# Optimization experiments

Hardware: AMD Instinct MI355X
Metric: run time of the kernel (lower is better)

## Reference

```python
import jax, jax.numpy as jnp
import numpy as np

N_NODES = 100000
N_EDGES = 1600000
NFEAT = 128
NHID = 128
NCLASS = 16


def _sage_conv(x, src, dst, w_self, w_neigh, b):
    # mean aggregation over in-neighbors: for each dst, mean of x[src]
    msgs = x[src]                                   # [E, F] gather
    agg = jax.ops.segment_sum(msgs, dst, num_segments=x.shape[0])  # [N, F]
    deg = jax.ops.segment_sum(jnp.ones((src.shape[0],), x.dtype), dst,
                              num_segments=x.shape[0])             # [N]
    h_neigh = agg / jnp.maximum(deg, 1.0)[:, None]
    return x @ w_self + h_neigh @ w_neigh + b


def setup_inputs() -> dict:
    key = jax.random.key(0)
    ks = jax.random.split(key, 9)
    x = jax.random.normal(ks[0], (N_NODES, NFEAT), dtype=jnp.float32)
    src = jax.random.randint(ks[1], (N_EDGES,), 0, N_NODES, dtype=jnp.int32)
    dst = jax.random.randint(ks[2], (N_EDGES,), 0, N_NODES, dtype=jnp.int32)
    s1 = 1.0 / np.sqrt(NFEAT)
    s2 = 1.0 / np.sqrt(NHID)
    w_self1 = jax.random.uniform(ks[3], (NFEAT, NHID), jnp.float32, -s1, s1)
    w_neigh1 = jax.random.uniform(ks[4], (NFEAT, NHID), jnp.float32, -s1, s1)
    b1 = jnp.zeros((NHID,), jnp.float32)
    w_self2 = jax.random.uniform(ks[5], (NHID, NCLASS), jnp.float32, -s2, s2)
    w_neigh2 = jax.random.uniform(ks[6], (NHID, NCLASS), jnp.float32, -s2, s2)
    b2 = jnp.zeros((NCLASS,), jnp.float32)
    return {"x": x, "src": src, "dst": dst,
            "w_self1": w_self1, "w_neigh1": w_neigh1, "b1": b1,
            "w_self2": w_self2, "w_neigh2": w_neigh2, "b2": b2}


def reference(x, src, dst, w_self1, w_neigh1, b1, w_self2, w_neigh2, b2):
    h = jax.nn.relu(_sage_conv(x, src, dst, w_self1, w_neigh1, b1))
    # dropout is identity in eval mode (training=False)
    out = _sage_conv(h, src, dst, w_self2, w_neigh2, b2)
    return jax.nn.log_softmax(out, axis=1)
```

## Files before the change

### kernel.cpp

```cpp
#include <hip/hip_runtime.h>
#include <math.h>

#define NN 100000
#define NE 1600000
#define BSZ 64
#define NBUCK ((NN + BSZ - 1) / BSZ)
#define NBLK 256
#define CHUNK ((NE + NBLK - 1) / NBLK)
#define NH (NBUCK * NBLK)
#define NSB ((NH + 1023) / 1024)

typedef unsigned int uint;
typedef unsigned short ushort_t;
typedef float f32x2 __attribute__((ext_vector_type(2)));
typedef float f32x4 __attribute__((ext_vector_type(4)));
typedef short s16x8 __attribute__((ext_vector_type(8)));

union U4S8 { uint4 u; s16x8 s; };

__device__ inline uint bf16_1(float f) {
  uint u = __float_as_uint(f);
  return (u + 0x7FFFu + ((u >> 16) & 1u)) >> 16;
}
__device__ inline uint bf16_2(float lo, float hi) {
  return bf16_1(lo) | (bf16_1(hi) << 16);
}
__device__ inline float blo(uint u) { return __uint_as_float(u << 16); }
__device__ inline float bhi(uint u) { return __uint_as_float(u & 0xFFFF0000u); }

__device__ inline f32x4 mfma_bf16(uint4 a, uint4 b, f32x4 c) {
  U4S8 ua, ub; ua.u = a; ub.u = b;
  return __builtin_amdgcn_mfma_f32_16x16x32_bf16(ua.s, ub.s, c, 0, 0, 0);
}

__global__ __launch_bounds__(256) void tobf16_kernel(
    const float* __restrict__ x, uint* __restrict__ xh,
    uint* __restrict__ xq) {
  int i = blockIdx.x * 256 + threadIdx.x;
  if (i >= NN * 16) return;
  const float4* p = (const float4*)x + (size_t)i * 2;
  float4 a = p[0], b = p[1];
  uint4 o;
  o.x = bf16_2(a.x, a.y);
  o.y = bf16_2(a.z, a.w);
  o.z = bf16_2(b.x, b.y);
  o.w = bf16_2(b.z, b.w);
  ((uint4*)xh)[i] = o;
  int q0 = __builtin_amdgcn_cvt_pk_fp8_f32(a.x, a.y, 0, false);
  q0 = __builtin_amdgcn_cvt_pk_fp8_f32(a.z, a.w, q0, true);
  int q1 = __builtin_amdgcn_cvt_pk_fp8_f32(b.x, b.y, 0, false);
  q1 = __builtin_amdgcn_cvt_pk_fp8_f32(b.z, b.w, q1, true);
  uint2 oq; oq.x = (uint)q0; oq.y = (uint)q1;
  int r = i >> 4;
  int u = (i & 15) * 2;
  *(uint2*)(xq + (size_t)r * 32 + u) = oq;
}

__global__ __launch_bounds__(256) void prep_w_kernel(
    const float* __restrict__ ws1, const float* __restrict__ wn1,
    const float* __restrict__ ws2, const float* __restrict__ wn2,
    uint* __restrict__ w1t, uint* __restrict__ w2t) {
  int idx = blockIdx.x * 256 + threadIdx.x;
  if (idx < 128 * 128) {
    int col = idx >> 7, ku = idx & 127;
    int k = ku * 2;
    const float* w = (k < 128) ? ws1 : wn1;
    int kk = (k < 128) ? k : (k - 128);
    w1t[idx] = bf16_2(w[(size_t)kk * 128 + col], w[(size_t)(kk + 1) * 128 + col]);
  } else if (idx < 128 * 128 + 32 * 64) {
    int j = idx - 128 * 128;
    int col = j >> 6, ku = j & 63;
    int k = ku * 2;
    const float* w = (col < 16) ? ws2 : wn2;
    int c = col & 15;
    w2t[j] = bf16_2(w[(size_t)k * 16 + c], w[(size_t)(k + 1) * 16 + c]);
  }
}

__global__ __launch_bounds__(1024) void histA_kernel(
    const int* __restrict__ dst, int* __restrict__ hist2) {
  __shared__ int lh[NBUCK];
  int tid = threadIdx.x;
  int b = blockIdx.x;
  for (int i = tid; i < NBUCK; i += 1024) lh[i] = 0;
  __syncthreads();
  int e0 = b * CHUNK, e1 = min(e0 + CHUNK, NE);
  for (int e = e0 + tid; e < e1; e += 1024) {
    atomicAdd(&lh[dst[e] >> 6], 1);
  }
  __syncthreads();
  for (int i = tid; i < NBUCK; i += 1024)
    hist2[(size_t)b * NBUCK + i] = lh[i];
}

__global__ __launch_bounds__(1024) void transpose_kernel(
    const int* __restrict__ hist2, int* __restrict__ hist) {
  __shared__ int t[32][33];
  int tx = threadIdx.x & 31, ty = threadIdx.x >> 5;
  int i = blockIdx.x * 32 + tx;
  int b = blockIdx.y * 32 + ty;
  if (i < NBUCK) t[ty][tx] = hist2[(size_t)b * NBUCK + i];
  __syncthreads();
  int i2 = blockIdx.x * 32 + ty;
  int b2 = blockIdx.y * 32 + tx;
  if (i2 < NBUCK) hist[(size_t)i2 * NBLK + b2] = t[tx][ty];
}

__global__ __launch_bounds__(1024) void scan_sums_kernel(
    const int* __restrict__ hist, int* __restrict__ sums) {
  __shared__ int sdata[1024];
  int i = blockIdx.x * 1024 + threadIdx.x;
  sdata[threadIdx.x] = (i < NH) ? hist[i] : 0;
  __syncthreads();
#pragma unroll
  for (int s = 512; s > 0; s >>= 1) {
    if (threadIdx.x < s) sdata[threadIdx.x] += sdata[threadIdx.x + s];
    __syncthreads();
  }
  if (threadIdx.x == 0) sums[blockIdx.x] = sdata[0];
}

__global__ __launch_bounds__(512) void scan_tops_kernel(int* __restrict__ sums) {
  __shared__ int buf[2][512];
  int tid = threadIdx.x;
  int v = (tid < NSB) ? sums[tid] : 0;
  buf[0][tid] = v;
  __syncthreads();
  int pp = 0;
#pragma unroll
  for (int d = 1; d < 512; d <<= 1) {
    buf[pp ^ 1][tid] = buf[pp][tid] + ((tid >= d) ? buf[pp][tid - d] : 0);
    pp ^= 1;
    __syncthreads();
  }
  if (tid < NSB) sums[tid] = buf[pp][tid] - v;
}

__global__ __launch_bounds__(1024) void scan_apply_kernel(
    int* __restrict__ hist, const int* __restrict__ sums) {
  __shared__ int buf[2][1024];
  int tid = threadIdx.x;
  int i = blockIdx.x * 1024 + tid;
  int v = (i < NH) ? hist[i] : 0;
  buf[0][tid] = v;
  __syncthreads();
  int pp = 0;
#pragma unroll
  for (int d = 1; d < 1024; d <<= 1) {
    buf[pp ^ 1][tid] = buf[pp][tid] + ((tid >= d) ? buf[pp][tid - d] : 0);
    pp ^= 1;
    __syncthreads();
  }
  if (i < NH) hist[i] = sums[blockIdx.x] + buf[pp][tid] - v;
}

__global__ __launch_bounds__(1024) void scatter3_kernel(
    const int* __restrict__ src, const int* __restrict__ dst,
    const int* __restrict__ scanned, unsigned int* __restrict__ ebuf) {
  __shared__ int cur[NBUCK];
  int tid = threadIdx.x;
  int b = blockIdx.x;
  for (int i = tid; i < NBUCK; i += 1024) cur[i] = scanned[i * NBLK + b];
  __syncthreads();
  int e0 = b * CHUNK, e1 = min(e0 + CHUNK, NE);
  for (int e = e0 + tid; e < e1; e += 1024) {
    int d = dst[e];
    int p = atomicAdd(&cur[d >> 6], 1);
    ebuf[p] = ((unsigned int)(d & 63) << 17) | (unsigned int)src[e];
  }
}

__global__ __launch_bounds__(256) void bucket_sort_kernel(
    const unsigned int* __restrict__ ebuf, const int* __restrict__ scanned,
    int* __restrict__ deg, int* __restrict__ off, int* __restrict__ perm) {
  __shared__ int cnt[BSZ];
  __shared__ int loc_off[BSZ];
  int tid = threadIdx.x;
  int b = blockIdx.x;
  int e0 = scanned[b * NBLK];
  int e1 = (b + 1 < NBUCK) ? scanned[(b + 1) * NBLK] : NE;

  if (tid < BSZ) cnt[tid] = 0;
  __syncthreads();
  for (int e = e0 + tid; e < e1; e += 256)
    atomicAdd(&cnt[ebuf[e] >> 17], 1);
  __syncthreads();

  if (tid < BSZ) {
    int v = cnt[tid];
    int incl = v;
#pragma unroll
    for (int d = 1; d < 64; d <<= 1) {
      int t = __shfl_up(incl, d);
      if (tid >= d) incl += t;
    }
    int excl = incl - v;
    loc_off[tid] = e0 + excl;
    int node = b * BSZ + tid;
    if (node < NN) { off[node] = e0 + excl; deg[node] = v; }
    cnt[tid] = 0;
  }
  __syncthreads();

  for (int e = e0 + tid; e < e1; e += 256) {
    unsigned int pk = ebuf[e];
    int dl = pk >> 17;
    int p = loc_off[dl] + atomicAdd(&cnt[dl], 1);
    perm[p] = (int)(pk & 0x1FFFF);
  }
}

__global__ __launch_bounds__(256) void mean1_kernel(
    const uint* __restrict__ xq, const int* __restrict__ off,
    const int* __restrict__ deg, const int* __restrict__ perm,
    uint* __restrict__ m1h) {
  int node = blockIdx.x * 4 + (threadIdx.x >> 6);
  int lane = threadIdx.x & 63;
  if (node >= NN) return;
  int o = off[node], dg = deg[node];
  int slot = lane >> 5;
  int q = lane & 31;
  f32x2 a0 = {0.f, 0.f}, a1 = {0.f, 0.f};
  int j = 0;
  for (; j + 8 <= dg; j += 8) {
    int sA = perm[o + j + slot];
    int sB = perm[o + j + 2 + slot];
    int sC = perm[o + j + 4 + slot];
    int sD = perm[o + j + 6 + slot];
    uint vA = xq[(size_t)sA * 32 + q];
    uint vB = xq[(size_t)sB * 32 + q];
    uint vC = xq[(size_t)sC * 32 + q];
    uint vD = xq[(size_t)sD * 32 + q];
    a0 += __builtin_amdgcn_cvt_pk_f32_fp8(vA, 0);
    a1 += __builtin_amdgcn_cvt_pk_f32_fp8(vA, 1);
    a0 += __builtin_amdgcn_cvt_pk_f32_fp8(vB, 0);
    a1 += __builtin_amdgcn_cvt_pk_f32_fp8(vB, 1);
    a0 += __builtin_amdgcn_cvt_pk_f32_fp8(vC, 0);
    a1 += __builtin_amdgcn_cvt_pk_f32_fp8(vC, 1);
    a0 += __builtin_amdgcn_cvt_pk_f32_fp8(vD, 0);
    a1 += __builtin_amdgcn_cvt_pk_f32_fp8(vD, 1);
  }
  for (; j + 2 <= dg; j += 2) {
    int s = perm[o + j + slot];
    uint v = xq[(size_t)s * 32 + q];
    a0 += __builtin_amdgcn_cvt_pk_f32_fp8(v, 0);
    a1 += __builtin_amdgcn_cvt_pk_f32_fp8(v, 1);
  }
  if (j < dg && slot == 0) {
    int s = perm[o + j];
    uint v = xq[(size_t)s * 32 + q];
    a0 += __builtin_amdgcn_cvt_pk_f32_fp8(v, 0);
    a1 += __builtin_amdgcn_cvt_pk_f32_fp8(v, 1);
  }
  a0.x += __shfl_xor(a0.x, 32);
  a0.y += __shfl_xor(a0.y, 32);
  a1.x += __shfl_xor(a1.x, 32);
  a1.y += __shfl_xor(a1.y, 32);
  if (slot == 0) {
    float rd = 1.0f / fmaxf((float)dg, 1.0f);
    uint2 o2;
    o2.x = bf16_2(a0.x * rd, a0.y * rd);
    o2.y = bf16_2(a1.x * rd, a1.y * rd);
    *(uint2*)(m1h + (size_t)node * 64 + q * 2) = o2;
  }
}

__global__ __launch_bounds__(256) void gemm12_kernel(
    const uint* __restrict__ xh, const uint* __restrict__ m1h,
    const uint* __restrict__ w1t, const uint* __restrict__ w2t,
    const float* __restrict__ b1, float* __restrict__ oself,
    ushort_t* __restrict__ h2b) {
  __shared__ uint lds_w[128 * 128];
  int tid = threadIdx.x;

#pragma unroll
  for (int i = 0; i < 16; i++) {
    int g = tid + i * 256;
    int row = g >> 5, c = g & 31;
    uint4 v = ((const uint4*)w1t)[g];
    int cs = c ^ (row & 7);
    *(uint4*)&lds_w[row * 128 + cs * 4] = v;
  }
  __syncthreads();

  int wv = tid >> 6;
  int lane = tid & 63;
  int lr = lane & 15, lk = lane >> 4;
  int r0 = blockIdx.x * 256 + wv * 64;

  f32x4 acc[4][8];
#pragma unroll
  for (int i = 0; i < 4; i++)
#pragma unroll
    for (int j = 0; j < 8; j++) acc[i][j] = (f32x4){0.f, 0.f, 0.f, 0.f};

#pragma unroll
  for (int ks = 0; ks < 8; ks++) {
    const uint* A = (ks < 4) ? xh : m1h;
    int ku = (ks & 3) * 16 + lk * 4;
    uint4 a[4];
#pragma unroll
    for (int rt = 0; rt < 4; rt++) {
      int row = r0 + rt * 16 + lr;
      if (row >= NN) row = NN - 1;
      a[rt] = *(const uint4*)(A + (size_t)row * 64 + ku);
    }
    int cbase = ks * 4 + lk;
#pragma unroll
    for (int ct = 0; ct < 8; ct++) {
      int brow = ct * 16 + lr;
      int cs = cbase ^ (lr & 7);
      uint4 bu = *(const uint4*)&lds_w[brow * 128 + cs * 4];
#pragma unroll
      for (int rt = 0; rt < 4; rt++)
        acc[rt][ct] = mfma_bf16(a[rt], bu, acc[rt][ct]);
    }
  }

  float bias[8];
#pragma unroll
  for (int ct = 0; ct < 8; ct++) bias[ct] = b1[ct * 16 + lr];

  __syncthreads();

  ushort_t* lds_h = (ushort_t*)lds_w;
#pragma unroll
  for (int rt = 0; rt < 4; rt++) {
#pragma unroll
    for (int r = 0; r < 4; r++) {
      int rel = wv * 64 + rt * 16 + lk * 4 + r;
#pragma unroll
      for (int ct = 0; ct < 8; ct++) {
        int col = ct * 16 + lr;
        float v = fmaxf(acc[rt][ct][r] + bias[ct], 0.0f);
        int chunk = col >> 3;
        int cs = chunk ^ ((rel & 7) << 1);
        lds_h[rel * 128 + (cs << 3) + (col & 7)] = (ushort_t)bf16_1(v);
      }
    }
  }

  f32x4 acc2[4][2];
#pragma unroll
  for (int i = 0; i < 4; i++)
#pragma unroll
    for (int j = 0; j < 2; j++) acc2[i][j] = (f32x4){0.f, 0.f, 0.f, 0.f};

#pragma unroll
  for (int ks = 0; ks < 4; ks++) {
    uint4 a[4];
#pragma unroll
    for (int rt = 0; rt < 4; rt++) {
      int rel = wv * 64 + rt * 16 + lr;
      int chunk = ks * 4 + lk;
      int cs = chunk ^ ((rel & 7) << 1);
      a[rt] = *(const uint4*)&lds_h[rel * 128 + (cs << 3)];
    }
#pragma unroll
    for (int ct = 0; ct < 2; ct++) {
      uint4 bu = *(const uint4*)(w2t + (size_t)(ct * 16 + lr) * 64 + ks * 16 + lk * 4);
      acc2[0][ct] = mfma_bf16(a[0], bu, acc2[0][ct]);
      acc2[1][ct] = mfma_bf16(a[1], bu, acc2[1][ct]);
      acc2[2][ct] = mfma_bf16(a[2], bu, acc2[2][ct]);
      acc2[3][ct] = mfma_bf16(a[3], bu, acc2[3][ct]);
    }
  }

#pragma unroll
  for (int rt = 0; rt < 4; rt++) {
#pragma unroll
    for (int r = 0; r < 4; r++) {
      int row = r0 + rt * 16 + lk * 4 + r;
      if (row < NN) {
        oself[(size_t)row * 16 + lr] = acc2[rt][0][r];
        h2b[(size_t)row * 16 + lr]  = (ushort_t)bf16_1(acc2[rt][1][r]);
      }
    }
  }
}

__global__ __launch_bounds__(256) void mean2_kernel(
    const ushort_t* __restrict__ h2b, const int* __restrict__ off,
    const int* __restrict__ deg, const int* __restrict__ perm,
    const float* __restrict__ oself, const float* __restrict__ b2,
    float* __restrict__ out) {
  int node = blockIdx.x * 4 + (threadIdx.x >> 6);
  int lane = threadIdx.x & 63;
  if (node >= NN) return;
  int o = off[node], dg = deg[node];
  int slot = lane >> 3;
  int q = lane & 7;
  const uint* hb = (const uint*)h2b;
  float a0 = 0.f, a1 = 0.f;
  int j = slot;
  for (; j + 8 < dg; j += 16) {
    int sA = perm[o + j];
    int sB = perm[o + j + 8];
    uint vA = hb[(size_t)sA * 8 + q];
    uint vB = hb[(size_t)sB * 8 + q];
    a0 += blo(vA) + blo(vB);
    a1 += bhi(vA) + bhi(vB);
  }
  if (j < dg) {
    int s = perm[o + j];
    uint v = hb[(size_t)s * 8 + q];
    a0 += blo(v);
    a1 += bhi(v);
  }
#pragma unroll
  for (int d = 8; d <= 32; d <<= 1) {
    a0 += __shfl_xor(a0, d);
    a1 += __shfl_xor(a1, d);
  }
  float rd = 1.0f / fmaxf((float)dg, 1.0f);
  float2 ob = *(const float2*)(b2 + q * 2);
  float2 os = *(const float2*)(oself + (size_t)node * 16 + q * 2);
  float l0 = os.x + ob.x + a0 * rd;
  float l1 = os.y + ob.y + a1 * rd;
  float m = fmaxf(l0, l1);
#pragma unroll
  for (int d = 1; d <= 4; d <<= 1) m = fmaxf(m, __shfl_xor(m, d));
  float s = __expf(l0 - m) + __expf(l1 - m);
#pragma unroll
  for (int d = 1; d <= 4; d <<= 1) s += __shfl_xor(s, d);
  if (slot == 0) {
    float ls = logf(s);
    float2 r;
    r.x = l0 - m - ls;
    r.y = l1 - m - ls;
    *(float2*)(out + (size_t)node * 16 + q * 2) = r;
  }
}

extern "C" void kernel_launch(void* const* d_in, const int* in_sizes, int n_in,
                              void* d_out, int out_size, void* d_ws, size_t ws_size,
                              hipStream_t stream) {
  const float* x   = (const float*)d_in[0];
  const int*   src = (const int*)d_in[1];
  const int*   dst = (const int*)d_in[2];
  const float* ws1 = (const float*)d_in[3];
  const float* wn1 = (const float*)d_in[4];
  const float* b1  = (const float*)d_in[5];
  const float* ws2 = (const float*)d_in[6];
  const float* wn2 = (const float*)d_in[7];
  const float* b2  = (const float*)d_in[8];
  float* out = (float*)d_out;

  char* p = (char*)d_ws;
  int* deg   = (int*)p;  p += (size_t)NN * 4;
  int* off   = (int*)p;  p += (size_t)NN * 4;
  int* hist  = (int*)p;  p += (size_t)NH * 4;
  int* hist2 = (int*)p;  p += (size_t)NH * 4;
  int* sums  = (int*)p;  p += (size_t)((NSB + 31) & ~31) * 4;
  unsigned int* ebuf = (unsigned int*)p; p += (size_t)NE * 4;
  int* perm = (int*)p;  p += (size_t)NE * 4;
  uint* xh   = (uint*)p; p += (size_t)NN * 64 * 4;
  uint* m1h  = (uint*)p; p += (size_t)NN * 64 * 4;
  uint* xq   = (uint*)p; p += (size_t)NN * 32 * 4;
  uint* w1t  = (uint*)p; p += (size_t)128 * 128 * 4;
  uint* w2t  = (uint*)p; p += (size_t)32 * 64 * 4;
  ushort_t* h2b = (ushort_t*)p; p += (size_t)NN * 16 * 2;
  float* osf    = (float*)p;    p += (size_t)NN * 16 * 4;

  tobf16_kernel<<<(NN * 16 + 255) / 256, 256, 0, stream>>>(x, xh, xq);
  prep_w_kernel<<<(128 * 128 + 32 * 64 + 255) / 256, 256, 0, stream>>>(
      ws1, wn1, ws2, wn2, w1t, w2t);

  histA_kernel<<<NBLK, 1024, 0, stream>>>(dst, hist2);
  transpose_kernel<<<dim3((NBUCK + 31) / 32, NBLK / 32), 1024, 0, stream>>>(
      hist2, hist);
  scan_sums_kernel<<<NSB, 1024, 0, stream>>>(hist, sums);
  scan_tops_kernel<<<1, 512, 0, stream>>>(sums);
  scan_apply_kernel<<<NSB, 1024, 0, stream>>>(hist, sums);
  scatter3_kernel<<<NBLK, 1024, 0, stream>>>(src, dst, hist, ebuf);
  bucket_sort_kernel<<<NBUCK, 256, 0, stream>>>(ebuf, hist, deg, off, perm);

  mean1_kernel<<<(NN + 3) / 4, 256, 0, stream>>>(xq, off, deg, perm, m1h);

  gemm12_kernel<<<(NN + 255) / 256, 256, 0, stream>>>(
      xh, m1h, w1t, w2t, b1, osf, h2b);

  mean2_kernel<<<(NN + 3) / 4, 256, 0, stream>>>(h2b, off, deg, perm, osf, b2, out);
}
```

Measured before the change: 170.1 us.

## Merge prep kernels, load GEMM weights via global_load_lds, process two row tiles per block

Combines the x conversion and weight-prep kernels into a single launch, removing one kernel launch. The gemm12 kernel now loads the weight matrix straight into LDS with global_load_lds, using a pre-swizzled source address, instead of staging it through registers. Each block now handles 512 rows in two halves, which halves the grid. It reloads W1 into LDS between the halves because the LDS buffer is reused for the hidden activations. The fewer blocks reduce per-block fixed overhead but may lower occupancy and parallelism, and the extra syncs and reload add cost.

After: 169.7 us. No clear change (-0.2%).

```diff
diff --git a/kernel.cpp b/kernel.cpp
--- a/kernel.cpp
+++ b/kernel.cpp
@@ -33,47 +33,45 @@
   return __builtin_amdgcn_mfma_f32_16x16x32_bf16(ua.s, ub.s, c, 0, 0, 0);
 }
 
-__global__ __launch_bounds__(256) void tobf16_kernel(
-    const float* __restrict__ x, uint* __restrict__ xh,
-    uint* __restrict__ xq) {
-  int i = blockIdx.x * 256 + threadIdx.x;
-  if (i >= NN * 16) return;
-  const float4* p = (const float4*)x + (size_t)i * 2;
-  float4 a = p[0], b = p[1];
-  uint4 o;
-  o.x = bf16_2(a.x, a.y);
-  o.y = bf16_2(a.z, a.w);
-  o.z = bf16_2(b.x, b.y);
-  o.w = bf16_2(b.z, b.w);
-  ((uint4*)xh)[i] = o;
-  int q0 = __builtin_amdgcn_cvt_pk_fp8_f32(a.x, a.y, 0, false);
-  q0 = __builtin_amdgcn_cvt_pk_fp8_f32(a.z, a.w, q0, true);
-  int q1 = __builtin_amdgcn_cvt_pk_fp8_f32(b.x, b.y, 0, false);
-  q1 = __builtin_amdgcn_cvt_pk_fp8_f32(b.z, b.w, q1, true);
-  uint2 oq; oq.x = (uint)q0; oq.y = (uint)q1;
-  int r = i >> 4;
-  int u = (i & 15) * 2;
-  *(uint2*)(xq + (size_t)r * 32 + u) = oq;
-}
-
-__global__ __launch_bounds__(256) void prep_w_kernel(
+__global__ __launch_bounds__(256) void prep_kernel(
+    const float* __restrict__ x, uint* __restrict__ xh, uint* __restrict__ xq,
     const float* __restrict__ ws1, const float* __restrict__ wn1,
     const float* __restrict__ ws2, const float* __restrict__ wn2,
     uint* __restrict__ w1t, uint* __restrict__ w2t) {
-  int idx = blockIdx.x * 256 + threadIdx.x;
-  if (idx < 128 * 128) {
-    int col = idx >> 7, ku = idx & 127;
-    int k = ku * 2;
-    const float* w = (k < 128) ? ws1 : wn1;
-    int kk = (k < 128) ? k : (k - 128);
-    w1t[idx] = bf16_2(w[(size_t)kk * 128 + col], w[(size_t)(kk + 1) * 128 + col]);
-  } else if (idx < 128 * 128 + 32 * 64) {
-    int j = idx - 128 * 128;
-    int col = j >> 6, ku = j & 63;
-    int k = ku * 2;
-    const float* w = (col < 16) ? ws2 : wn2;
-    int c = col & 15;
-    w2t[j] = bf16_2(w[(size_t)k * 16 + c], w[(size_t)(k + 1) * 16 + c]);
+  int i = blockIdx.x * 256 + threadIdx.x;
+  if (i < NN * 16) {
+    const float4* p = (const float4*)x + (size_t)i * 2;
+    float4 a = p[0], b = p[1];
+    uint4 o;
+    o.x = bf16_2(a.x, a.y);
+    o.y = bf16_2(a.z, a.w);
+    o.z = bf16_2(b.x, b.y);
+    o.w = bf16_2(b.z, b.w);
+    ((uint4*)xh)[i] = o;
+    int q0 = __builtin_amdgcn_cvt_pk_fp8_f32(a.x, a.y, 0, false);
+    q0 = __builtin_amdgcn_cvt_pk_fp8_f32(a.z, a.w, q0, true);
+    int q1 = __builtin_amdgcn_cvt_pk_fp8_f32(b.x, b.y, 0, false);
+    q1 = __builtin_amdgcn_cvt_pk_fp8_f32(b.z, b.w, q1, true);
+    uint2 oq; oq.x = (uint)q0; oq.y = (uint)q1;
+    int r = i >> 4;
+    int u = (i & 15) * 2;
+    *(uint2*)(xq + (size_t)r * 32 + u) = oq;
+  } else {
+    int idx = i - NN * 16;
+    if (idx < 128 * 128) {
+      int col = idx >> 7, ku = idx & 127;
+      int k = ku * 2;
+      const float* w = (k < 128) ? ws1 : wn1;
+      int kk = (k < 128) ? k : (k - 128);
+      w1t[idx] = bf16_2(w[(size_t)kk * 128 + col], w[(size_t)(kk + 1) * 128 + col]);
+    } else if (idx < 128 * 128 + 32 * 64) {
+      int j = idx - 128 * 128;
+      int col = j >> 6, ku = j & 63;
+      int k = ku * 2;
+      const float* w = (col < 16) ? ws2 : wn2;
+      int c = col & 15;
+      w2t[j] = bf16_2(w[(size_t)k * 16 + c], w[(size_t)(k + 1) * 16 + c]);
+    }
   }
 }
 
@@ -272,109 +270,127 @@
     ushort_t* __restrict__ h2b) {
   __shared__ uint lds_w[128 * 128];
   int tid = threadIdx.x;
-
-#pragma unroll
-  for (int i = 0; i < 16; i++) {
-    int g = tid + i * 256;
-    int row = g >> 5, c = g & 31;
-    uint4 v = ((const uint4*)w1t)[g];
-    int cs = c ^ (row & 7);
-    *(uint4*)&lds_w[row * 128 + cs * 4] = v;
-  }
-  __syncthreads();
-
   int wv = tid >> 6;
   int lane = tid & 63;
+
+  {
+#pragma unroll
+    for (int i = 0; i < 16; i++) {
+      int g = tid + i * 256;
+      int row = g >> 5, cs = g & 31;
+      int gsrc = row * 32 + (cs ^ (row & 7));
+      __builtin_amdgcn_global_load_lds(
+          (const uint*)((const uint4*)w1t + gsrc),
+          &lds_w[(size_t)(wv * 64 + i * 256) * 4], 16, 0, 0);
+    }
+  }
+  __syncthreads();
+
   int lr = lane & 15, lk = lane >> 4;
-  int r0 = blockIdx.x * 256 + wv * 64;
-
-  f32x4 acc[4][8];
-#pragma unroll
-  for (int i = 0; i < 4; i++)
-#pragma unroll
-    for (int j = 0; j < 8; j++) acc[i][j] = (f32x4){0.f, 0.f, 0.f, 0.f};
-
-#pragma unroll
-  for (int ks = 0; ks < 8; ks++) {
-    const uint* A = (ks < 4) ? xh : m1h;
-    int ku = (ks & 3) * 16 + lk * 4;
-    uint4 a[4];
+  float bias[8];
+#pragma unroll
+  for (int ct = 0; ct < 8; ct++) bias[ct] = b1[ct * 16 + lr];
+
+  for (int half = 0; half < 2; half++) {
+    int r0 = blockIdx.x * 512 + half * 256 + wv * 64;
+
+    f32x4 acc[4][8];
+#pragma unroll
+    for (int i = 0; i < 4; i++)
+#pragma unroll
+      for (int j = 0; j < 8; j++) acc[i][j] = (f32x4){0.f, 0.f, 0.f, 0.f};
+
+#pragma unroll
+    for (int ks = 0; ks < 8; ks++) {
+      const uint* A = (ks < 4) ? xh : m1h;
+      int ku = (ks & 3) * 16 + lk * 4;
+      uint4 a[4];
+#pragma unroll
+      for (int rt = 0; rt < 4; rt++) {
+        int row = r0 + rt * 16 + lr;
+        if (row >= NN) row = NN - 1;
+        a[rt] = *(const uint4*)(A + (size_t)row * 64 + ku);
+      }
+      int cbase = ks * 4 + lk;
+#pragma unroll
+      for (int ct = 0; ct < 8; ct++) {
+        int brow = ct * 16 + lr;
+        int cs = cbase ^ (lr & 7);
+        uint4 bu = *(const uint4*)&lds_w[brow * 128 + cs * 4];
+#pragma unroll
+        for (int rt = 0; rt < 4; rt++)
+          acc[rt][ct] = mfma_bf16(a[rt], bu, acc[rt][ct]);
+      }
+    }
+
+    __syncthreads();
+    ushort_t* lds_h = (ushort_t*)lds_w;
 #pragma unroll
     for (int rt = 0; rt < 4; rt++) {
-      int row = r0 + rt * 16 + lr;
-      if (row >= NN) row = NN - 1;
-      a[rt] = *(const uint4*)(A + (size_t)row * 64 + ku);
-    }
-    int cbase = ks * 4 + lk;
-#pragma unroll
-    for (int ct = 0; ct < 8; ct++) {
-      int brow = ct * 16 + lr;
-      int cs = cbase ^ (lr & 7);
-      uint4 bu = *(const uint4*)&lds_w[brow * 128 + cs * 4];
-#pragma unroll
-      for (int rt = 0; rt < 4; rt++)
-        acc[rt][ct] = mfma_bf16(a[rt], bu, acc[rt][ct]);
-    }
-  }
-
-  float bias[8];
-#pragma unroll
-  for (int ct = 0; ct < 8; ct++) bias[ct] = b1[ct * 16 + lr];
-
-  __syncthreads();
-
-  ushort_t* lds_h = (ushort_t*)lds_w;
-#pragma unroll
-  for (int rt = 0; rt < 4; rt++) {
-#pragma unroll
-    for (int r = 0; r < 4; r++) {
-      int rel = wv * 64 + rt * 16 + lk * 4 + r;
-#pragma unroll
-      for (int ct = 0; ct < 8; ct++) {
-        int col = ct * 16 + lr;
-        float v = fmaxf(acc[rt][ct][r] + bias[ct], 0.0f);
-        int chunk = col >> 3;
+#pragma unroll
+      for (int r = 0; r < 4; r++) {
+        int rel = wv * 64 + rt * 16 + lk * 4 + r;
+#pragma unroll
+        for (int ct = 0; ct < 8; ct++) {
+          int col = ct * 16 + lr;
+          float v = fmaxf(acc[rt][ct][r] + bias[ct], 0.0f);
+          int chunk = col >> 3;
+          int cs = chunk ^ ((rel & 7) << 1);
+          lds_h[rel * 128 + (cs << 3) + (col & 7)] = (ushort_t)bf16_1(v);
+        }
+      }
+    }
+
+    f32x4 acc2[4][2];
+#pragma unroll
+    for (int i = 0; i < 4; i++)
+#pragma unroll
+      for (int j = 0; j < 2; j++) acc2[i][j] = (f32x4){0.f, 0.f, 0.f, 0.f};
+
+#pragma unroll
+    for (int ks = 0; ks < 4; ks++) {
+      uint4 a[4];
+#pragma unroll
+      for (int rt = 0; rt < 4; rt++) {
+        int rel = wv * 64 + rt * 16 + lr;
+        int chunk = ks * 4 + lk;
         int cs = chunk ^ ((rel & 7) << 1);
-        lds_h[rel * 128 + (cs << 3) + (col & 7)] = (ushort_t)bf16_1(v);
-      }
-    }
-  }
-
-  f32x4 acc2[4][2];
-#pragma unroll
-  for (int i = 0; i < 4; i++)
-#pragma unroll
-    for (int j = 0; j < 2; j++) acc2[i][j] = (f32x4){0.f, 0.f, 0.f, 0.f};
-
-#pragma unroll
-  for (int ks = 0; ks < 4; ks++) {
-    uint4 a[4];
+        a[rt] = *(const uint4*)&lds_h[rel * 128 + (cs << 3)];
+      }
+#pragma unroll
+      for (int ct = 0; ct < 2; ct++) {
+        uint4 bu = *(const uint4*)(w2t + (size_t)(ct * 16 + lr) * 64 + ks * 16 + lk * 4);
+        acc2[0][ct] = mfma_bf16(a[0], bu, acc2[0][ct]);
+        acc2[1][ct] = mfma_bf16(a[1], bu, acc2[1][ct]);
+        acc2[2][ct] = mfma_bf16(a[2], bu, acc2[2][ct]);
+        acc2[3][ct] = mfma_bf16(a[3], bu, acc2[3][ct]);
+      }
+    }
+
 #pragma unroll
     for (int rt = 0; rt < 4; rt++) {
-      int rel = wv * 64 + rt * 16 + lr;
-      int chunk = ks * 4 + lk;
-      int cs = chunk ^ ((rel & 7) << 1);
-      a[rt] = *(const uint4*)&lds_h[rel * 128 + (cs << 3)];
-    }
-#pragma unroll
-    for (int ct = 0; ct < 2; ct++) {
-      uint4 bu = *(const uint4*)(w2t + (size_t)(ct * 16 + lr) * 64 + ks * 16 + lk * 4);
-      acc2[0][ct] = mfma_bf16(a[0], bu, acc2[0][ct]);
-      acc2[1][ct] = mfma_bf16(a[1], bu, acc2[1][ct]);
-      acc2[2][ct] = mfma_bf16(a[2], bu, acc2[2][ct]);
-      acc2[3][ct] = mfma_bf16(a[3], bu, acc2[3][ct]);
-    }
-  }
-
-#pragma unroll
-  for (int rt = 0; rt < 4; rt++) {
-#pragma unroll
-    for (int r = 0; r < 4; r++) {
-      int row = r0 + rt * 16 + lk * 4 + r;
-      if (row < NN) {
-        oself[(size_t)row * 16 + lr] = acc2[rt][0][r];
-        h2b[(size_t)row * 16 + lr]  = (ushort_t)bf16_1(acc2[rt][1][r]);
-      }
+#pragma unroll
+      for (int r = 0; r < 4; r++) {
+        int row = r0 + rt * 16 + lk * 4 + r;
+        if (row < NN) {
+          oself[(size_t)row * 16 + lr] = acc2[rt][0][r];
+          h2b[(size_t)row * 16 + lr]  = (ushort_t)bf16_1(acc2[rt][1][r]);
+        }
+      }
+    }
+
+    if (half == 0) {
+      __syncthreads();
+#pragma unroll
+      for (int i = 0; i < 16; i++) {
+        int g = tid + i * 256;
+        int row = g >> 5, cs = g & 31;
+        int gsrc = row * 32 + (cs ^ (row & 7));
+        __builtin_amdgcn_global_load_lds(
+            (const uint*)((const uint4*)w1t + gsrc),
+            &lds_w[(size_t)(wv * 64 + i * 256) * 4], 16, 0, 0);
+      }
+      __syncthreads();
     }
   }
 }
@@ -462,9 +478,8 @@
   ushort_t* h2b = (ushort_t*)p; p += (size_t)NN * 16 * 2;
   float* osf    = (float*)p;    p += (size_t)NN * 16 * 4;
 
-  tobf16_kernel<<<(NN * 16 + 255) / 256, 256, 0, stream>>>(x, xh, xq);
-  prep_w_kernel<<<(128 * 128 + 32 * 64 + 255) / 256, 256, 0, stream>>>(
-      ws1, wn1, ws2, wn2, w1t, w2t);
+  prep_kernel<<<(NN * 16 + 128 * 128 + 32 * 64 + 255) / 256, 256, 0, stream>>>(
+      x, xh, xq, ws1, wn1, ws2, wn2, w1t, w2t);
 
   histA_kernel<<<NBLK, 1024, 0, stream>>>(dst, hist2);
   transpose_kernel<<<dim3((NBUCK + 31) / 32, NBLK / 32), 1024, 0, stream>>>(
@@ -477,7 +492,7 @@
 
   mean1_kernel<<<(NN + 3) / 4, 256, 0, stream>>>(xq, off, deg, perm, m1h);
 
-  gemm12_kernel<<<(NN + 255) / 256, 256, 0, stream>>>(
+  gemm12_kernel<<<(NN + 511) / 512, 256, 0, stream>>>(
       xh, m1h, w1t, w2t, b1, osf, h2b);
 
   mean2_kernel<<<(NN + 3) / 4, 256, 0, stream>>>(h2b, off, deg, perm, osf, b2, out);
```
